# Kernel tuning notes

Measured on AMD Instinct MI355X. Metric: run time of the kernel, lower is better.

The kernel has to match this reference:

```python
import jax, jax.numpy as jnp
import numpy as np

N_NODES = 10000
IN_CH = 128
OUT_CH = 256
N_EDGES = 320000
K = 16  # neighbors


def setup_inputs() -> dict:
    key = jax.random.key(0)
    k1, k2, k3 = jax.random.split(key, 3)
    x = jax.random.normal(k1, (N_NODES, IN_CH), dtype=jnp.float32)
    edge_index = jax.random.randint(k2, (2, N_EDGES), 0, N_NODES, dtype=jnp.int32)
    W = jax.random.normal(k3, (IN_CH, OUT_CH), dtype=jnp.float32) * 0.05
    b = jnp.zeros((OUT_CH,), dtype=jnp.float32)
    return {"x": x, "edge_index": edge_index, "W": W, "b": b}


def _knn_edges(x, k):
    # torch_geometric knn_graph(x, k, loop=False): edge (neighbor -> node)
    n = x.shape[0]
    sq = jnp.sum(x * x, axis=1)
    dist = sq[:, None] + sq[None, :] - 2.0 * (x @ x.T)  # [N, N]
    dist = dist.at[jnp.arange(n), jnp.arange(n)].set(jnp.inf)  # no self-loops
    _, nbr = jax.lax.top_k(-dist, k)  # [N, k] indices of k nearest
    src = nbr.reshape(-1).astype(jnp.int32)          # neighbors (sources)
    tgt = jnp.repeat(jnp.arange(n, dtype=jnp.int32), k)  # query nodes (targets)
    return src, tgt


def reference(x, edge_index, W, b):
    n = x.shape[0]
    # --- dynamic kNN graph ---
    src, tgt = _knn_edges(x, K)
    # --- dedup: replicate remove_duplicated_edges exactly (asymmetric bases) ---
    max1 = edge_index.max() + 1
    key1 = edge_index[1] * max1 + edge_index[0]
    max2 = jnp.maximum(src.max(), tgt.max()) + 1
    key2 = tgt * max2 + src
    dup = jnp.isin(key2, key1)
    # removing a duplicated edge == giving it weight 0 in GCN (deg + aggregation)
    knn_w = (~dup).astype(x.dtype)
    loops = jnp.arange(n, dtype=jnp.int32)
    row = jnp.concatenate([edge_index[0], src, loops])
    col = jnp.concatenate([edge_index[1], tgt, loops])
    ew = jnp.concatenate([
        jnp.ones((edge_index.shape[1],), x.dtype),
        knn_w,
        jnp.ones((n,), x.dtype),  # self-loop weight (GCNConv fill_value=1)
    ])
    # --- GCNConv: symmetric normalization D^-1/2 A D^-1/2 ---
    deg = jax.ops.segment_sum(ew, col, num_segments=n)
    dinv = jnp.where(deg > 0, jax.lax.rsqrt(deg), 0.0)
    norm = dinv[row] * ew * dinv[col]  # per-edge coefficient
    h = x @ W  # [N, OUT_CH]
    agg = jax.ops.segment_sum(norm[:, None] * h[row], col, num_segments=n)
    return jax.nn.relu(agg + b)
```

## Files before the change

### kernel.cpp

```cpp
#include <hip/hip_runtime.h>
#include <hip/hip_fp16.h>
#include <math.h>

#define IN_CH 128
#define OUT_CH 256
#define KNN 16
#define HASH_BITS 20
#define HASH_SIZE (1 << HASH_BITS)
#define HASH_MASK (HASH_SIZE - 1)
#define CAP 128
#define BINCAP 32
#define JSPL 8
#define SWEEP_QT 64
#define SWEEP_JT 64

using short8v = __attribute__((ext_vector_type(8))) short;
using f32x4   = __attribute__((ext_vector_type(4))) float;

__device__ __forceinline__ unsigned hashk(int key) {
    return ((unsigned)key * 2654435761u) & HASH_MASK;
}

__device__ __forceinline__ unsigned short f2bf(float f) {
    union { float f; unsigned u; } v; v.f = f;
    unsigned r = v.u + 0x7fff + ((v.u >> 16) & 1);
    return (unsigned short)(r >> 16);
}

__device__ __forceinline__ unsigned f2h(float f) {
    return (unsigned)__half_as_ushort(__float2half_rn(f));
}
__device__ __forceinline__ float h2f(unsigned h) {
    return __half2float(__ushort_as_half((unsigned short)h));
}

__device__ __forceinline__ void stage16(const void* g, void* l) {
    __builtin_amdgcn_global_load_lds(
        (const __attribute__((address_space(1))) unsigned int*)g,
        (__attribute__((address_space(3))) unsigned int*)l, 16, 0, 0);
}

__global__ __launch_bounds__(256)
void prep_kernel(const float* __restrict__ x, const int* __restrict__ ei,
                 unsigned short* __restrict__ xbt, unsigned short* __restrict__ xb,
                 float* __restrict__ sq, float* __restrict__ statp,
                 float* __restrict__ statp2, int* __restrict__ dmaxp,
                 int* __restrict__ degns, int* __restrict__ cnt,
                 int* __restrict__ hash, int N, int n2) {
    __shared__ float red[8];
    __shared__ int redi[4];
    int t = threadIdx.x;
    int lane = t & 63, w = t >> 6;
    int row = blockIdx.x * 16 + (t >> 4);
    int seg = t & 15;
    int gid = blockIdx.x * 256 + t;
    int tot = gridDim.x * 256;
    if (gid < N) { degns[gid] = 0; cnt[gid] = 0; }
    for (int i = gid; i < HASH_SIZE; i += tot) hash[i] = -1;
    float s = 0.f;
    if (row < N) {
        const float* rp = x + (size_t)row * IN_CH + seg * 8;
        float4 a = *(const float4*)rp;
        float4 b = *(const float4*)(rp + 4);
        s = a.x * a.x + a.y * a.y + a.z * a.z + a.w * a.w
          + b.x * b.x + b.y * b.y + b.z * b.z + b.w * b.w;
        union { unsigned short u[8]; uint4 v; } o;
        o.u[0] = f2bf(a.x); o.u[1] = f2bf(a.y); o.u[2] = f2bf(a.z); o.u[3] = f2bf(a.w);
        o.u[4] = f2bf(b.x); o.u[5] = f2bf(b.y); o.u[6] = f2bf(b.z); o.u[7] = f2bf(b.w);
        *(uint4*)(xbt + (size_t)(row >> 6) * 8192 + seg * 512 + (row & 63) * 8) = o.v;
        *(uint4*)(xb + (size_t)row * IN_CH + seg * 8) = o.v;
    }
#pragma unroll
    for (int off = 8; off > 0; off >>= 1) s += __shfl_xor(s, off, 16);
    float s1 = 0.f, s2 = 0.f;
    if (seg == 0 && row < N) { sq[row] = s; s1 = s; s2 = s * s; }
#pragma unroll
    for (int off = 32; off > 0; off >>= 1) {
        s1 += __shfl_xor(s1, off, 64);
        s2 += __shfl_xor(s2, off, 64);
    }
    int m = 0;
    for (int i = gid; i < n2; i += tot) m = max(m, ei[i]);
#pragma unroll
    for (int off = 32; off > 0; off >>= 1) m = max(m, __shfl_xor(m, off, 64));
    if (lane == 0) { red[w] = s1; red[4 + w] = s2; redi[w] = m; }
    __syncthreads();
    if (t == 0) {
        statp[blockIdx.x]  = red[0] + red[1] + red[2] + red[3];
        statp2[blockIdx.x] = red[4] + red[5] + red[6] + red[7];
        dmaxp[blockIdx.x]  = max(max(redi[0], redi[1]), max(redi[2], redi[3]));
    }
}

__global__ __launch_bounds__(256, 4)
void mid_kernel(const unsigned short* __restrict__ xbt, const float* __restrict__ sq,
                const float* __restrict__ statp, const float* __restrict__ statp2,
                const int* __restrict__ dmaxp, const int* __restrict__ ei,
                int* __restrict__ hash, int* __restrict__ degns,
                int* __restrict__ cnt, unsigned* __restrict__ cand,
                int N, int chunkA, int nsw, int nprep, int E) {
    __shared__ unsigned short buf[2][SWEEP_JT * IN_CH];
    __shared__ unsigned binj[SWEEP_QT * BINCAP];
    __shared__ int bcnt[SWEEP_QT];
    __shared__ int bases[SWEEP_QT];
    __shared__ float sred[8];
    __shared__ int mred[4];

    const int tid = threadIdx.x;
    const int lane = tid & 63;
    const int w = tid >> 6;

    if (blockIdx.x >= nsw) {
        int m = 0;
        for (int i = tid; i < nprep; i += 256) m = max(m, dmaxp[i]);
#pragma unroll
        for (int off = 32; off > 0; off >>= 1) m = max(m, __shfl_xor(m, off, 64));
        if (lane == 0) mred[w] = m;
        __syncthreads();
        int max1 = max(max(mred[0], mred[1]), max(mred[2], mred[3])) + 1;
        int e = (blockIdx.x - nsw) * 256 + tid;
        if (e >= E) return;
        int e0 = ei[e], e1 = ei[E + e];
        int key = e1 * max1 + e0;
        unsigned p = hashk(key);
        while (true) {
            int prev = atomicCAS(&hash[p], -1, key);
            if (prev == -1 || prev == key) break;
            p = (p + 1) & HASH_MASK;
        }
        atomicAdd(&degns[e1], 1);
        return;
    }

    const int qb = blockIdx.x >> 3;
    const int split = blockIdx.x & 7;
    const int q0 = qb * SWEEP_QT;
    const int js = split * chunkA;
    const int je = min(N, js + chunkA);
    const int l15 = lane & 15, kg = lane >> 4;
    const int kg4 = kg * 4;

    float s1 = 0.f, s2 = 0.f;
    for (int i = tid; i < nprep; i += 256) { s1 += statp[i]; s2 += statp2[i]; }
#pragma unroll
    for (int off = 32; off > 0; off >>= 1) {
        s1 += __shfl_xor(s1, off, 64);
        s2 += __shfl_xor(s2, off, 64);
    }
    if (lane == 0) { sred[w] = s1; sred[4 + w] = s2; }
    if (tid < SWEEP_QT) bcnt[tid] = 0;
    __syncthreads();
    const float mean = (sred[0] + sred[1] + sred[2] + sred[3]) / N;
    const float var  = (sred[4] + sred[5] + sred[6] + sred[7]) / N - mean * mean;

    short8v A[4];
    {
        int gq = q0 + w * 16 + l15; if (gq >= N) gq = N - 1;
        const unsigned short* rb = xbt + (size_t)(gq >> 6) * 8192 + (gq & 63) * 8;
#pragma unroll
        for (int s = 0; s < 4; s++) A[s] = *(const short8v*)(rb + (s * 4 + kg) * 512);
    }
    float negT2[4];
#pragma unroll
    for (int r = 0; r < 4; r++) {
        int gq = q0 + w * 16 + kg4 + r;
        negT2[r] = (gq < N)
            ? -0.5f * (mean - 2.5f * sqrtf(var + 4.f * sq[gq]) + 1.0f)
            : 3e30f;
    }

    const int nt = (je > js) ? (je - js + SWEEP_JT - 1) / SWEEP_JT : 0;

#define STAGE(tl, bsel) {                                                       \
    const char* sb = (const char*)xbt + (size_t)((js + (tl) * SWEEP_JT) >> 6) * 16384; \
    _Pragma("unroll")                                                           \
    for (int it = 0; it < 4; it++) {                                            \
        int g = w * 4 + it;                                                     \
        stage16(sb + g * 1024 + lane * 16, (char*)&buf[bsel][0] + g * 1024);    \
    }                                                                           \
}

    if (nt > 0) STAGE(0, 0)
    int cur = 0;
    for (int tile = 0; tile < nt; tile++) {
        int jt0 = js + tile * SWEEP_JT;
        if (tile + 1 < nt) {
            STAGE(tile + 1, cur ^ 1)
            asm volatile("s_waitcnt vmcnt(4)" ::: "memory");
        } else {
            asm volatile("s_waitcnt vmcnt(0)" ::: "memory");
        }
        __builtin_amdgcn_s_barrier();
        __builtin_amdgcn_sched_barrier(0);
        const char* bb = (const char*)&buf[cur][0];
        f32x4 acc[4];
#pragma unroll
        for (int jf = 0; jf < 4; jf++) {
            int jr = jt0 + jf * 16 + l15; int cj = jr < N ? jr : N - 1;
            float iv = -0.5f * sq[cj];
            acc[jf] = (f32x4){iv, iv, iv, iv};
        }
#pragma unroll
        for (int ks = 0; ks < 4; ks++) {
            int coff = (ks * 4 + kg) * 1024 + l15 * 16;
#pragma unroll
            for (int jf = 0; jf < 4; jf++) {
                short8v B = *(const short8v*)(bb + coff + jf * 256);
                acc[jf] = __builtin_amdgcn_mfma_f32_16x16x32_bf16(A[ks], B, acc[jf], 0, 0, 0);
            }
        }
#pragma unroll
        for (int jf = 0; jf < 4; jf++) {
            int gj = jt0 + jf * 16 + l15;
            bool jok = gj < je;
#pragma unroll
            for (int r = 0; r < 4; r++) {
                if (jok && acc[jf][r] > negT2[r]) {
                    int ql = w * 16 + kg4 + r;
                    if (q0 + ql != gj) {
                        unsigned d16 = f2h(-2.0f * acc[jf][r]);
                        int p = atomicAdd(&bcnt[ql], 1);
                        if (p < BINCAP) binj[ql * BINCAP + p] = (d16 << 16) | (unsigned)gj;
                    }
                }
            }
        }
        __builtin_amdgcn_sched_barrier(0);
        __builtin_amdgcn_s_barrier();
        cur ^= 1;
    }
#undef STAGE

    __syncthreads();
    if (tid < SWEEP_QT) {
        int gq = q0 + tid;
        int c = min(bcnt[tid], BINCAP);
        bcnt[tid] = c;
        bases[tid] = (gq < N && c > 0) ? atomicAdd(&cnt[gq], c) : 0;
    }
    __syncthreads();
    for (int ql = w; ql < SWEEP_QT; ql += 4) {
        int gq = q0 + ql;
        if (gq >= N) continue;
        int c = bcnt[ql], base = bases[ql];
        if (lane < c) {
            int pos = base + lane;
            if (pos < CAP) cand[(size_t)gq * CAP + pos] = binj[ql * BINCAP + lane];
        }
    }
}

__global__ __launch_bounds__(256)
void refine_scan_kernel(const float* __restrict__ x, const float* __restrict__ sq,
                        const int* __restrict__ cnt, const unsigned* __restrict__ cand,
                        const int* __restrict__ hash, int* __restrict__ nbr,
                        int* __restrict__ knnw, const int* __restrict__ degns,
                        float* __restrict__ dinv, int* __restrict__ offs,
                        int* __restrict__ curs, int nrq, int N) {
    __shared__ float dist[4][CAP];
    __shared__ unsigned short vlist[4][CAP];
    __shared__ int wsum2[4], wbase2[4];
    int tid = threadIdx.x;
    int w = tid >> 6, lane = tid & 63;

    if (blockIdx.x == (unsigned)nrq) {
        int CH = (N + 255) / 256;
        int c0 = tid * CH;
        int s = 0;
        for (int i = 0; i < CH; i++) {
            int idx = c0 + i;
            if (idx < N) s += degns[idx];
        }
        int incl = s;
#pragma unroll
        for (int o = 1; o < 64; o <<= 1) {
            int v = __shfl_up(incl, o, 64);
            if (lane >= o) incl += v;
        }
        if (lane == 63) wsum2[w] = incl;
        __syncthreads();
        if (tid == 0) {
            int run = 0;
#pragma unroll
            for (int i = 0; i < 4; i++) { wbase2[i] = run; run += wsum2[i]; }
            offs[N] = run;
        }
        __syncthreads();
        int run = wbase2[w] + incl - s;
        for (int i = 0; i < CH; i++) {
            int idx = c0 + i;
            if (idx < N) { offs[idx] = run; curs[idx] = run; run += degns[idx]; }
        }
        return;
    }

    int q = blockIdx.x * 4 + w;
    if (q >= N) return;
    int nc = min(cnt[q], CAP);
    int grp = lane >> 4, gl = lane & 15;

    float aA[2]; int jA[2];
#pragma unroll
    for (int s = 0; s < 2; s++) {
        int idx = lane + s * 64;
        aA[s] = INFINITY; jA[s] = 0x7fffffff;
        if (idx < nc) {
            unsigned cv = cand[(size_t)q * CAP + idx];
            jA[s] = (int)(cv & 0xFFFFu);
            aA[s] = h2f(cv >> 16);
        }
    }
    float thr = INFINITY;
    {
        float aa[2] = {aA[0], aA[1]}; int jj[2] = {jA[0], jA[1]};
        float d = INFINITY; int j2 = 0x7fffffff;
        for (int k = 0; k < KNN; k++) {
            d = aa[0]; j2 = jj[0];
            if (aa[1] < d || (aa[1] == d && jj[1] < j2)) { d = aa[1]; j2 = jj[1]; }
            for (int o = 32; o > 0; o >>= 1) {
                float od = __shfl_xor(d, o, 64); int oj = __shfl_xor(j2, o, 64);
                if (od < d || (od == d && oj < j2)) { d = od; j2 = oj; }
            }
#pragma unroll
            for (int s = 0; s < 2; s++)
                if (aa[s] == d && jj[s] == j2) aa[s] = INFINITY;
        }
        if (j2 != 0x7fffffff) thr = d + 0.75f;
    }
    int cs = 0;
#pragma unroll
    for (int s = 0; s < 2; s++) {
        bool p = (lane + s * 64 < nc) && (aA[s] <= thr);
        unsigned long long m = __ballot(p);
        int pre = __popcll(m & ((1ull << lane) - 1ull));
        if (p) vlist[w][cs + pre] = (unsigned short)jA[s];
        cs += __popcll(m);
    }
    const float4* rq4 = (const float4*)(x + (size_t)q * IN_CH);
    float4 a0 = rq4[gl], a1 = rq4[gl + 16];
    for (int c = grp; c < cs; c += 4) {
        int j = vlist[w][c];
        const float4* rj4 = (const float4*)(x + (size_t)j * IN_CH);
        float4 b0 = rj4[gl], b1 = rj4[gl + 16];
        float p = a0.x * b0.x + a0.y * b0.y + a0.z * b0.z + a0.w * b0.w
                + a1.x * b1.x + a1.y * b1.y + a1.z * b1.z + a1.w * b1.w;
#pragma unroll
        for (int o = 8; o > 0; o >>= 1) p += __shfl_xor(p, o, 16);
        if (gl == 0) dist[w][c] = sq[j] - 2.f * p;
    }
    float dex[2]; int jB[2];
#pragma unroll
    for (int s = 0; s < 2; s++) {
        int idx = lane + s * 64;
        dex[s] = INFINITY; jB[s] = 0x7fffffff;
        if (idx < cs) { jB[s] = vlist[w][idx]; dex[s] = dist[w][idx]; }
    }
    int myj = q;
    for (int k = 0; k < KNN; k++) {
        float d = dex[0]; int j2 = jB[0];
        if (dex[1] < d || (dex[1] == d && jB[1] < j2)) { d = dex[1]; j2 = jB[1]; }
        for (int o = 32; o > 0; o >>= 1) {
            float od = __shfl_xor(d, o, 64); int oj = __shfl_xor(j2, o, 64);
            if (od < d || (od == d && oj < j2)) { d = od; j2 = oj; }
        }
        int jsel = (j2 == 0x7fffffff) ? q : j2;
        if (lane == k) myj = jsel;
#pragma unroll
        for (int s = 0; s < 2; s++)
            if (dex[s] == d && jB[s] == j2) dex[s] = INFINITY;
    }
    int wv = 0;
    if (lane < KNN) {
        int key = q * N + myj;
        unsigned p = hashk(key);
        wv = 1;
        while (true) {
            int v = hash[p];
            if (v == key) { wv = 0; break; }
            if (v == -1) break;
            p = (p + 1) & HASH_MASK;
        }
        nbr[(size_t)q * KNN + lane] = myj;
        knnw[(size_t)q * KNN + lane] = wv;
    }
    unsigned long long m = __ballot(lane < KNN && wv);
    if (lane == 0) dinv[q] = rsqrtf((float)(degns[q] + __popcll(m) + 1));
}

__global__ __launch_bounds__(256)
void fill_kernel(const int* __restrict__ ei, int* __restrict__ curs,
                 int* __restrict__ rows, int E) {
    int e = blockIdx.x * 256 + threadIdx.x;
    if (e >= E) return;
    int e0 = ei[e], e1 = ei[E + e];
    int pos = atomicAdd(&curs[e1], 1);
    rows[pos] = e0;
}

__global__ __launch_bounds__(256)
void gather_x(const int* __restrict__ offs, const int* __restrict__ rows,
              const int* __restrict__ nbr, const int* __restrict__ knnw,
              const float* __restrict__ dinv, const float* __restrict__ x,
              const unsigned short* __restrict__ xb, float* __restrict__ ax, int N) {
    int w = threadIdx.x >> 6, lane = threadIdx.x & 63;
    int n = blockIdx.x * 4 + w;
    if (n >= N) return;
    const float2* x2 = (const float2*)x;
    const unsigned* xbr = (const unsigned*)xb;
    int e0 = offs[n], e1 = offs[n + 1];
    int no = e1 - e0;
    int tot = no + KNN;
    float dvn = dinv[n];
    float2 xv = x2[(size_t)n * 64 + lane];
    float2 acc = make_float2(dvn * xv.x, dvn * xv.y);
    for (int base = 0; base < tot; base += 64) {
        int cnt2 = min(64, tot - base);
        int idx = base + lane;
        int r = 0; float dv = 0.f;
        if (idx < tot) {
            if (idx < no) { r = rows[e0 + idx]; dv = dinv[r]; }
            else {
                int k = idx - no;
                r = nbr[(size_t)n * KNN + k];
                dv = knnw[(size_t)n * KNN + k] ? dinv[r] : 0.f;
            }
        }
#pragma unroll 4
        for (int t = 0; t < cnt2; t++) {
            int rr = __shfl(r, t, 64);
            float dd = __shfl(dv, t, 64);
            unsigned v = xbr[(size_t)rr * 64 + lane];
            float lo = __uint_as_float(v << 16);
            float hi = __uint_as_float(v & 0xFFFF0000u);
            acc.x = fmaf(dd, lo, acc.x); acc.y = fmaf(dd, hi, acc.y);
        }
    }
    float2 o;
    o.x = dvn * acc.x; o.y = dvn * acc.y;
    ((float2*)ax)[(size_t)n * 64 + lane] = o;
}

__global__ __launch_bounds__(256)
void gemm_out(const float* __restrict__ ax, const float* __restrict__ W,
              const float* __restrict__ b, float* __restrict__ out, int N) {
    __shared__ float xs[32][IN_CH];
    int r0 = blockIdx.x * 32;
    int t = threadIdx.x;
#pragma unroll
    for (int i = t; i < 32 * 32; i += 256) {
        int r = i >> 5, c4 = (i & 31) * 4;
        float4 v = make_float4(0.f, 0.f, 0.f, 0.f);
        if (r0 + r < N) v = *(const float4*)(ax + (size_t)(r0 + r) * IN_CH + c4);
        *(float4*)&xs[r][c4] = v;
    }
    __syncthreads();
    float acc[32];
#pragma unroll
    for (int r = 0; r < 32; r++) acc[r] = 0.f;
    for (int c = 0; c < IN_CH; c++) {
        float wv = W[(size_t)c * OUT_CH + t];
#pragma unroll
        for (int r = 0; r < 32; r++) acc[r] = fmaf(xs[r][c], wv, acc[r]);
    }
    float bb = b[t];
#pragma unroll
    for (int r = 0; r < 32; r++)
        if (r0 + r < N) out[(size_t)(r0 + r) * OUT_CH + t] = fmaxf(acc[r] + bb, 0.f);
}

extern "C" void kernel_launch(void* const* d_in, const int* in_sizes, int n_in,
                              void* d_out, int out_size, void* d_ws, size_t ws_size,
                              hipStream_t stream) {
    const float* x = (const float*)d_in[0];
    const int* ei = (const int*)d_in[1];
    const float* W = (const float*)d_in[2];
    const float* b = (const float*)d_in[3];
    float* out = (float*)d_out;
    const int N = in_sizes[0] / IN_CH;
    const int E = in_sizes[1] / 2;

    char* P = (char*)d_ws;
    size_t o = 0;
    auto A_ = [&](size_t bytes) -> void* {
        void* p = P + o;
        o += (bytes + 255) & ~(size_t)255;
        return p;
    };
    const int nrb = (N + 63) / 64;
    const int nprep = (N + 15) / 16;
    float* sq    = (float*)A_((size_t)nrb * 64 * 4);
    unsigned short* xbt = (unsigned short*)A_((size_t)nrb * 16384);
    unsigned short* xb  = (unsigned short*)A_((size_t)N * IN_CH * 2);
    float* statp  = (float*)A_((size_t)nprep * 4);
    float* statp2 = (float*)A_((size_t)nprep * 4);
    int*   dmaxp  = (int*)A_((size_t)nprep * 4);
    int*   nbr   = (int*)A_((size_t)N * KNN * 4);
    int*   knnw  = (int*)A_((size_t)N * KNN * 4);
    int*   degns = (int*)A_((size_t)N * 4);
    float* dinv  = (float*)A_((size_t)N * 4);
    int*   offs  = (int*)A_((size_t)(N + 1) * 4);
    int*   curs  = (int*)A_((size_t)N * 4);
    int*   hash  = (int*)A_((size_t)HASH_SIZE * 4);
    size_t scratch = o;
    int*      cnt  = (int*)(P + scratch);
    unsigned* cand = (unsigned*)(P + scratch + 0x10000);
    float* ax   = (float*)(P + scratch);
    int*   rows = (int*)(P + scratch + (size_t)N * IN_CH * 4 + 0x10000);

    prep_kernel<<<nprep, 256, 0, stream>>>(x, ei, xbt, xb, sq, statp, statp2, dmaxp,
                                           degns, cnt, hash, N, 2 * E);
    int nqb = (N + SWEEP_QT - 1) / SWEEP_QT;
    int nsw = nqb * JSPL;
    int nins = (E + 255) / 256;
    int chunkA = (((N + JSPL - 1) / JSPL) + SWEEP_JT - 1) / SWEEP_JT * SWEEP_JT;
    mid_kernel<<<nsw + nins, 256, 0, stream>>>(xbt, sq, statp, statp2, dmaxp, ei,
                                               hash, degns, cnt, cand,
                                               N, chunkA, nsw, nprep, E);
    int nrq = (N + 3) / 4;
    refine_scan_kernel<<<nrq + 1, 256, 0, stream>>>(x, sq, cnt, cand, hash, nbr, knnw,
                                                    degns, dinv, offs, curs, nrq, N);
    fill_kernel<<<(E + 255) / 256, 256, 0, stream>>>(ei, curs, rows, E);
    gather_x<<<(N + 3) / 4, 256, 0, stream>>>(offs, rows, nbr, knnw, dinv, x, xb, ax, N);
    gemm_out<<<(N + 31) / 32, 256, 0, stream>>>(ax, W, b, out, N);
}
```

Baseline: 253.0 us.

## Fuse neighbor gather and output GEMM into one kernel via shared memory

Merges the aggregation kernel and the dense GEMM so each block gathers 16 nodes' normalized features into LDS and immediately multiplies by W with bias and ReLU. This removes the intermediate ax buffer write/read and one kernel launch. In exchange, each block now reuses W over 16 rows instead of 32, increasing total W reads, and the gather phase runs with fewer parallel waves per node group.

New measurement: 256.8 us. No clear change (+1.5%).

```diff
diff --git a/kernel.cpp b/kernel.cpp
--- a/kernel.cpp
+++ b/kernel.cpp
@@ -398,74 +398,67 @@
 }
 
 __global__ __launch_bounds__(256)
-void gather_x(const int* __restrict__ offs, const int* __restrict__ rows,
-              const int* __restrict__ nbr, const int* __restrict__ knnw,
-              const float* __restrict__ dinv, const float* __restrict__ x,
-              const unsigned short* __restrict__ xb, float* __restrict__ ax, int N) {
-    int w = threadIdx.x >> 6, lane = threadIdx.x & 63;
-    int n = blockIdx.x * 4 + w;
-    if (n >= N) return;
+void gather_gemm(const int* __restrict__ offs, const int* __restrict__ rows,
+                 const int* __restrict__ nbr, const int* __restrict__ knnw,
+                 const float* __restrict__ dinv, const float* __restrict__ x,
+                 const unsigned short* __restrict__ xb, const float* __restrict__ W,
+                 const float* __restrict__ b, float* __restrict__ out, int N) {
+    __shared__ float axs[16][IN_CH];
+    int tid = threadIdx.x;
+    int w = tid >> 6, lane = tid & 63;
+    int r0 = blockIdx.x * 16;
     const float2* x2 = (const float2*)x;
     const unsigned* xbr = (const unsigned*)xb;
-    int e0 = offs[n], e1 = offs[n + 1];
-    int no = e1 - e0;
-    int tot = no + KNN;
-    float dvn = dinv[n];
-    float2 xv = x2[(size_t)n * 64 + lane];
-    float2 acc = make_float2(dvn * xv.x, dvn * xv.y);
-    for (int base = 0; base < tot; base += 64) {
-        int cnt2 = min(64, tot - base);
-        int idx = base + lane;
-        int r = 0; float dv = 0.f;
-        if (idx < tot) {
-            if (idx < no) { r = rows[e0 + idx]; dv = dinv[r]; }
-            else {
-                int k = idx - no;
-                r = nbr[(size_t)n * KNN + k];
-                dv = knnw[(size_t)n * KNN + k] ? dinv[r] : 0.f;
+
+#pragma unroll
+    for (int i = 0; i < 4; i++) {
+        int n = r0 + w * 4 + i;
+        if (n >= N) break;
+        int e0 = offs[n], e1 = offs[n + 1];
+        int no = e1 - e0;
+        int tot = no + KNN;
+        float dvn = dinv[n];
+        float2 xv = x2[(size_t)n * 64 + lane];
+        float2 acc = make_float2(dvn * xv.x, dvn * xv.y);
+        for (int base = 0; base < tot; base += 64) {
+            int cnt2 = min(64, tot - base);
+            int idx = base + lane;
+            int r = 0; float dv = 0.f;
+            if (idx < tot) {
+                if (idx < no) { r = rows[e0 + idx]; dv = dinv[r]; }
+                else {
+                    int k = idx - no;
+                    r = nbr[(size_t)n * KNN + k];
+                    dv = knnw[(size_t)n * KNN + k] ? dinv[r] : 0.f;
+                }
             }
-        }
 #pragma unroll 4
-        for (int t = 0; t < cnt2; t++) {
-            int rr = __shfl(r, t, 64);
-            float dd = __shfl(dv, t, 64);
-            unsigned v = xbr[(size_t)rr * 64 + lane];
-            float lo = __uint_as_float(v << 16);
-            float hi = __uint_as_float(v & 0xFFFF0000u);
-            acc.x = fmaf(dd, lo, acc.x); acc.y = fmaf(dd, hi, acc.y);
-        }
-    }
-    float2 o;
-    o.x = dvn * acc.x; o.y = dvn * acc.y;
-    ((float2*)ax)[(size_t)n * 64 + lane] = o;
-}
-
-__global__ __launch_bounds__(256)
-void gemm_out(const float* __restrict__ ax, const float* __restrict__ W,
-              const float* __restrict__ b, float* __restrict__ out, int N) {
-    __shared__ float xs[32][IN_CH];
-    int r0 = blockIdx.x * 32;
-    int t = threadIdx.x;
-#pragma unroll
-    for (int i = t; i < 32 * 32; i += 256) {
-        int r = i >> 5, c4 = (i & 31) * 4;
-        float4 v = make_float4(0.f, 0.f, 0.f, 0.f);
-        if (r0 + r < N) v = *(const float4*)(ax + (size_t)(r0 + r) * IN_CH + c4);
-        *(float4*)&xs[r][c4] = v;
+            for (int t = 0; t < cnt2; t++) {
+                int rr = __shfl(r, t, 64);
+                float dd = __shfl(dv, t, 64);
+                unsigned v = xbr[(size_t)rr * 64 + lane];
+                float lo = __uint_as_float(v << 16);
+                float hi = __uint_as_float(v & 0xFFFF0000u);
+                acc.x = fmaf(dd, lo, acc.x); acc.y = fmaf(dd, hi, acc.y);
+            }
+        }
+        axs[w * 4 + i][lane * 2]     = dvn * acc.x;
+        axs[w * 4 + i][lane * 2 + 1] = dvn * acc.y;
     }
     __syncthreads();
-    float acc[32];
-#pragma unroll
-    for (int r = 0; r < 32; r++) acc[r] = 0.f;
+
+    float acc[16];
+#pragma unroll
+    for (int r = 0; r < 16; r++) acc[r] = 0.f;
     for (int c = 0; c < IN_CH; c++) {
-        float wv = W[(size_t)c * OUT_CH + t];
-#pragma unroll
-        for (int r = 0; r < 32; r++) acc[r] = fmaf(xs[r][c], wv, acc[r]);
-    }
-    float bb = b[t];
-#pragma unroll
-    for (int r = 0; r < 32; r++)
-        if (r0 + r < N) out[(size_t)(r0 + r) * OUT_CH + t] = fmaxf(acc[r] + bb, 0.f);
+        float wv = W[(size_t)c * OUT_CH + tid];
+#pragma unroll
+        for (int r = 0; r < 16; r++) acc[r] = fmaf(axs[r][c], wv, acc[r]);
+    }
+    float bb = b[tid];
+#pragma unroll
+    for (int r = 0; r < 16; r++)
+        if (r0 + r < N) out[(size_t)(r0 + r) * OUT_CH + tid] = fmaxf(acc[r] + bb, 0.f);
 }
 
 extern "C" void kernel_launch(void* const* d_in, const int* in_sizes, int n_in,
@@ -504,8 +497,7 @@
     size_t scratch = o;
     int*      cnt  = (int*)(P + scratch);
     unsigned* cand = (unsigned*)(P + scratch + 0x10000);
-    float* ax   = (float*)(P + scratch);
-    int*   rows = (int*)(P + scratch + (size_t)N * IN_CH * 4 + 0x10000);
+    int* rows = (int*)(P + scratch);
 
     prep_kernel<<<nprep, 256, 0, stream>>>(x, ei, xbt, xb, sq, statp, statp2, dmaxp,
                                            degns, cnt, hash, N, 2 * E);
@@ -520,6 +512,6 @@
     refine_scan_kernel<<<nrq + 1, 256, 0, stream>>>(x, sq, cnt, cand, hash, nbr, knnw,
                                                     degns, dinv, offs, curs, nrq, N);
     fill_kernel<<<(E + 255) / 256, 256, 0, stream>>>(ei, curs, rows, E);
-    gather_x<<<(N + 3) / 4, 256, 0, stream>>>(offs, rows, nbr, knnw, dinv, x, xb, ax, N);
-    gemm_out<<<(N + 31) / 32, 256, 0, stream>>>(ax, W, b, out, N);
-}
+    gather_gemm<<<(N + 15) / 16, 256, 0, stream>>>(offs, rows, nbr, knnw, dinv,
+                                                   x, xb, W, b, out, N);
+}
```
